# Performance work log

Measured on AMD Instinct MI355X. Metric: run time of the kernel, lower is better.

Reference implementation:

```python
import jax, jax.numpy as jnp
import numpy as np

HID = 512
NOISE = 128
VOCAB = 5000
BATCH = 256
STEPS = 64
EPS = 1e-5
SOS = VOCAB - 1

def lrelu(x):
    return jnp.where(x >= 0, x, 0.2 * x)

def batchnorm(x, gamma, beta):
    # training-mode BatchNorm1d: batch statistics, biased variance
    mu = jnp.mean(x, axis=0)
    var = jnp.mean((x - mu) ** 2, axis=0)
    return gamma * (x - mu) / jnp.sqrt(var + EPS) + beta

def gru_cell(x, h, w_ih, w_hh, b_ih, b_hh):
    gi = x @ w_ih.T + b_ih  # [B, 3H]
    gh = h @ w_hh.T + b_hh
    i_r, i_z, i_n = jnp.split(gi, 3, axis=1)
    h_r, h_z, h_n = jnp.split(gh, 3, axis=1)
    r = jax.nn.sigmoid(i_r + h_r)
    zg = jax.nn.sigmoid(i_z + h_z)
    n = jnp.tanh(i_n + r * h_n)
    return (1.0 - zg) * n + zg * h

def setup_inputs() -> dict:
    key = jax.random.key(0)
    ks = jax.random.split(key, 12)
    s = lambda fi, fo: 1.0 / np.sqrt(fi)
    u = lambda k, shp, b: jax.random.uniform(k, shp, jnp.float32, -b, b)
    return {
        "z": jax.random.normal(ks[0], (BATCH, NOISE), jnp.float32),
        "z2h_w": u(ks[1], (HID, NOISE), s(NOISE, HID)),
        "z2h_b": u(ks[2], (HID,), s(NOISE, HID)),
        "emb": jax.random.normal(ks[3], (VOCAB, HID), jnp.float32),
        "bn1_g": jnp.ones((HID,), jnp.float32), "bn1_b": jnp.zeros((HID,), jnp.float32),
        "bn2_g": jnp.ones((2 * HID,), jnp.float32), "bn2_b": jnp.zeros((2 * HID,), jnp.float32),
        "bn3_g": jnp.ones((HID,), jnp.float32), "bn3_b": jnp.zeros((HID,), jnp.float32),
        "gru_wih": u(ks[4], (3 * HID, 2 * HID), s(HID, 0)),
        "gru_whh": u(ks[5], (3 * HID, HID), s(HID, 0)),
        "gru_bih": u(ks[6], (3 * HID,), s(HID, 0)),
        "gru_bhh": u(ks[7], (3 * HID,), s(HID, 0)),
        "h2o_w": u(ks[8], (VOCAB, HID), s(HID, 0)),
        "h2o_b": u(ks[9], (VOCAB,), s(HID, 0)),
        "gumbel_u": jax.random.uniform(ks[10], (STEPS, BATCH, VOCAB), jnp.float32),
        "num_steps": STEPS,
        "temperature": 0.8,
    }

def reference(z, z2h_w, z2h_b, emb, bn1_g, bn1_b, bn2_g, bn2_b, bn3_g, bn3_b,
              gru_wih, gru_whh, gru_bih, gru_bhh, h2o_w, h2o_b, gumbel_u,
              num_steps, temperature):
    z0 = batchnorm(lrelu(z @ z2h_w.T + z2h_b), bn1_g, bn1_b)  # [B, H]
    h0 = z0
    prev0 = jnp.full((z.shape[0],), SOS, jnp.int32)

    def step(carry, u_t):
        h, prev = carry
        e = lrelu(emb[prev])                                   # [B, H]
        si = batchnorm(jnp.concatenate([e, z0], axis=1), bn2_g, bn2_b)
        h = gru_cell(si, h, gru_wih, gru_whh, gru_bih, gru_bhh)
        o = batchnorm(lrelu(h), bn3_g, bn3_b)
        logits = o @ h2o_w.T + h2o_b                           # [B, V]
        g = -jnp.log(-jnp.log(u_t + 1e-20) + 1e-20)            # gumbel noise
        y = jax.nn.softmax((logits + g) / temperature, axis=-1)
        prev = jnp.argmax(y, axis=-1).astype(jnp.int32)
        return (h, prev), y

    _, ys = jax.lax.scan(step, (h0, prev0), gumbel_u[:num_steps])
    return jnp.transpose(ys, (1, 0, 2))  # [B, steps, V]
```

## Files before the change

kernel.cpp:

```cpp
#include <hip/hip_runtime.h>
#include <math.h>

#define HH 512
#define BB 256
#define NK 128

__device__ __forceinline__ float lrelu(float x){ return x >= 0.f ? x : 0.2f*x; }
__device__ __forceinline__ float sigm(float x){ return 1.f/(1.f+expf(-x)); }

__device__ __forceinline__ float blk_sum(float v, float* red){
  int t = threadIdx.x;
  red[t] = v; __syncthreads();
  #pragma unroll
  for (int s = 128; s > 0; s >>= 1){
    if (t < s) red[t] += red[t+s];
    __syncthreads();
  }
  float r = red[0]; __syncthreads();
  return r;
}

__global__ __launch_bounds__(256) void k_init(
    const float* __restrict__ z, const float* __restrict__ w, const float* __restrict__ bz,
    const float* __restrict__ g1, const float* __restrict__ b1,
    const float* __restrict__ g2, const float* __restrict__ b2,
    float* __restrict__ h0, float* __restrict__ sz0, int* __restrict__ prev, int sos)
{
  __shared__ float red[256];
  int j = blockIdx.x, i = threadIdx.x;
  const float4* zr = (const float4*)(z + i*NK);
  const float4* wr = (const float4*)(w + j*NK);
  float acc = bz[j];
  #pragma unroll 8
  for (int k = 0; k < NK/4; k++){
    float4 a = zr[k], b = wr[k];
    acc = fmaf(a.x, b.x, acc); acc = fmaf(a.y, b.y, acc);
    acc = fmaf(a.z, b.z, acc); acc = fmaf(a.w, b.w, acc);
  }
  float t = lrelu(acc);
  float mu  = blk_sum(t, red) * (1.f/BB);
  float d   = t - mu;
  float var = blk_sum(d*d, red) * (1.f/BB);
  float z0v = g1[j] * d / sqrtf(var + 1e-5f) + b1[j];
  h0[i*HH + j] = z0v;
  float mu2  = blk_sum(z0v, red) * (1.f/BB);
  float d2   = z0v - mu2;
  float var2 = blk_sum(d2*d2, red) * (1.f/BB);
  sz0[i*HH + j] = g2[HH + j] * d2 / sqrtf(var2 + 1e-5f) + b2[HH + j];
  if (j == 0) prev[i] = sos;
}

__global__ __launch_bounds__(256) void k_embed(
    const int* __restrict__ prev, const float* __restrict__ emb,
    const float* __restrict__ g2, const float* __restrict__ b2,
    float* __restrict__ se)
{
  __shared__ float red[256];
  int j = blockIdx.x, i = threadIdx.x;
  float t = lrelu(emb[prev[i]*HH + j]);
  float mu  = blk_sum(t, red) * (1.f/BB);
  float d   = t - mu;
  float var = blk_sum(d*d, red) * (1.f/BB);
  se[i*HH + j] = g2[j] * d / sqrtf(var + 1e-5f) + b2[j];
}

__global__ __launch_bounds__(256) void k_bn3(
    const float* __restrict__ h, const float* __restrict__ g3, const float* __restrict__ b3,
    float* __restrict__ o)
{
  __shared__ float red[256];
  int j = blockIdx.x, i = threadIdx.x;
  float t = lrelu(h[i*HH + j]);
  float mu  = blk_sum(t, red) * (1.f/BB);
  float d   = t - mu;
  float var = blk_sum(d*d, red) * (1.f/BB);
  o[i*HH + j] = g3[j] * d / sqrtf(var + 1e-5f) + b3[j];
}

#define KT 64
__global__ __launch_bounds__(256) void k_gru(
    const float* __restrict__ se, const float* __restrict__ hcur,
    const float* __restrict__ wih, const float* __restrict__ whh,
    const float* __restrict__ gz0, const float* __restrict__ bhh,
    float* __restrict__ hnext)
{
  __shared__ float sA[2][32][68];
  __shared__ float sB[6][16][68];
  int m0 = blockIdx.x*32, kc0 = blockIdx.y*16;
  int tl = threadIdx.x;
  float accI[3][2] = {{0,0},{0,0},{0,0}};
  float accH[3][2] = {{0,0},{0,0},{0,0}};
  int c = tl & 15, r2 = (tl >> 4) * 2;

  for (int kt = 0; kt < HH; kt += KT){
    #pragma unroll
    for (int rep = 0; rep < 4; rep++){
      int f = tl + 256*rep;
      int mat = f >> 9; int fi = f & 511;
      int row = fi >> 4; int kq = (fi & 15) * 4;
      const float* src = mat ? hcur : se;
      *(float4*)&sA[mat][row][kq] = *(const float4*)&src[(m0+row)*HH + kt + kq];
    }
    #pragma unroll
    for (int rep = 0; rep < 6; rep++){
      int f = tl + 256*rep;
      int m6 = f >> 8; int fi = f & 255;
      int row = fi >> 4; int kq = (fi & 15) * 4;
      int gate = (m6 < 3) ? m6 : m6 - 3;
      int n = gate*HH + kc0 + row;
      float4 v;
      if (m6 < 3) v = *(const float4*)&wih[n*1024 + kt + kq];
      else        v = *(const float4*)&whh[n*HH   + kt + kq];
      *(float4*)&sB[m6][row][kq] = v;
    }
    __syncthreads();
    #pragma unroll
    for (int kk = 0; kk < KT; kk += 4){
      float4 a0 = *(const float4*)&sA[0][r2  ][kk];
      float4 a1 = *(const float4*)&sA[0][r2+1][kk];
      float4 h0v = *(const float4*)&sA[1][r2  ][kk];
      float4 h1v = *(const float4*)&sA[1][r2+1][kk];
      #pragma unroll
      for (int g = 0; g < 3; g++){
        float4 we = *(const float4*)&sB[g][c][kk];
        accI[g][0] = fmaf(a0.x,we.x, fmaf(a0.y,we.y, fmaf(a0.z,we.z, fmaf(a0.w,we.w, accI[g][0]))));
        accI[g][1] = fmaf(a1.x,we.x, fmaf(a1.y,we.y, fmaf(a1.z,we.z, fmaf(a1.w,we.w, accI[g][1]))));
        float4 wh = *(const float4*)&sB[3+g][c][kk];
        accH[g][0] = fmaf(h0v.x,wh.x, fmaf(h0v.y,wh.y, fmaf(h0v.z,wh.z, fmaf(h0v.w,wh.w, accH[g][0]))));
        accH[g][1] = fmaf(h1v.x,wh.x, fmaf(h1v.y,wh.y, fmaf(h1v.z,wh.z, fmaf(h1v.w,wh.w, accH[g][1]))));
      }
    }
    __syncthreads();
  }
  int k = kc0 + c;
  #pragma unroll
  for (int r = 0; r < 2; r++){
    int i = m0 + r2 + r;
    float gir = accI[0][r] + gz0[i*1536 + k];
    float giz = accI[1][r] + gz0[i*1536 + 512 + k];
    float gin = accI[2][r] + gz0[i*1536 + 1024 + k];
    float ghr = accH[0][r] + bhh[k];
    float ghz = accH[1][r] + bhh[512 + k];
    float ghn = accH[2][r] + bhh[1024 + k];
    float rg = sigm(gir + ghr);
    float zg = sigm(giz + ghz);
    float ng = tanhf(gin + rg*ghn);
    float hv = hcur[i*HH + k];
    hnext[i*HH + k] = (1.f - zg)*ng + zg*hv;
  }
}

__global__ __launch_bounds__(256) void k_mm(
    const float* __restrict__ A, int lda,
    const float* __restrict__ Bm, int ldb,
    const float* __restrict__ bias, int N,
    float* __restrict__ out, int ldc,
    int mode,
    const float* __restrict__ gum, int ldg,
    const float* __restrict__ temp)
{
  __shared__ float sA[32][68];
  __shared__ float sB[64][68];
  int m0 = blockIdx.x*32, n0 = blockIdx.y*64;
  int tl = threadIdx.x;
  float acc[4][2] = {{0,0},{0,0},{0,0},{0,0}};
  int c1 = tl & 31, r4 = (tl >> 5) * 4;

  for (int kt = 0; kt < HH; kt += 64){
    #pragma unroll
    for (int rep = 0; rep < 2; rep++){
      int f = tl + 256*rep; int row = f >> 4; int kq = (f & 15) * 4;
      *(float4*)&sA[row][kq] = *(const float4*)&A[(m0+row)*lda + kt + kq];
    }
    #pragma unroll
    for (int rep = 0; rep < 4; rep++){
      int f = tl + 256*rep; int row = f >> 4; int kq = (f & 15) * 4;
      float4 v = make_float4(0.f,0.f,0.f,0.f);
      if (n0 + row < N) v = *(const float4*)&Bm[(n0+row)*ldb + kt + kq];
      *(float4*)&sB[row][kq] = v;
    }
    __syncthreads();
    #pragma unroll
    for (int kk = 0; kk < 64; kk += 4){
      float4 b0 = *(const float4*)&sB[c1     ][kk];
      float4 b1 = *(const float4*)&sB[c1 + 32][kk];
      #pragma unroll
      for (int r = 0; r < 4; r++){
        float4 a = *(const float4*)&sA[r4+r][kk];
        acc[r][0] = fmaf(a.x,b0.x, fmaf(a.y,b0.y, fmaf(a.z,b0.z, fmaf(a.w,b0.w, acc[r][0]))));
        acc[r][1] = fmaf(a.x,b1.x, fmaf(a.y,b1.y, fmaf(a.z,b1.z, fmaf(a.w,b1.w, acc[r][1]))));
      }
    }
    __syncthreads();
  }

  if (mode == 0){
    #pragma unroll
    for (int r = 0; r < 4; r++)
      #pragma unroll
      for (int j = 0; j < 2; j++){
        int v = n0 + c1 + 32*j;
        if (v < N) out[(m0+r4+r)*ldc + v] = acc[r][j] + bias[v];
      }
  } else {
    float tv = temp[0];
    #pragma unroll
    for (int r = 0; r < 4; r++)
      #pragma unroll
      for (int j = 0; j < 2; j++){
        int v = n0 + c1 + 32*j;
        if (v < N){
          int i = m0 + r4 + r;
          float u = gum[i*ldg + v];
          float g = -logf(-logf(u + 1e-20f) + 1e-20f);
          out[i*ldc + v] = (acc[r][j] + bias[v] + g) / tv;
        }
      }
  }
}

__global__ __launch_bounds__(256) void k_softmax(
    float* __restrict__ outrow, int ldc, int V, int* __restrict__ prev)
{
  __shared__ float sbuf[5000];
  __shared__ float rmax[256];
  __shared__ int   ridx[256];
  __shared__ float rsum[256];
  int i = blockIdx.x, t = threadIdx.x;
  float* row = outrow + (long)i*ldc;
  float bm = -3.4e38f; int bi = 0;
  for (int v = t; v < V; v += 256){
    float s = row[v]; sbuf[v] = s;
    if (s > bm){ bm = s; bi = v; }
  }
  rmax[t] = bm; ridx[t] = bi; __syncthreads();
  for (int s = 128; s > 0; s >>= 1){
    if (t < s){
      float mv = rmax[t+s]; int mi = ridx[t+s];
      if (mv > rmax[t] || (mv == rmax[t] && mi < ridx[t])){ rmax[t] = mv; ridx[t] = mi; }
    }
    __syncthreads();
  }
  float m = rmax[0];
  float ls = 0.f;
  for (int v = t; v < V; v += 256){
    float p = expf(sbuf[v] - m); sbuf[v] = p; ls += p;
  }
  rsum[t] = ls; __syncthreads();
  for (int s = 128; s > 0; s >>= 1){
    if (t < s) rsum[t] += rsum[t+s];
    __syncthreads();
  }
  float inv = 1.f / rsum[0];
  for (int v = t; v < V; v += 256) row[v] = sbuf[v] * inv;
  if (t == 0) prev[i] = ridx[0];
}

extern "C" void kernel_launch(void* const* d_in, const int* in_sizes, int n_in,
                              void* d_out, int out_size, void* d_ws, size_t ws_size,
                              hipStream_t stream)
{
  const float* z     = (const float*)d_in[0];
  const float* z2h_w = (const float*)d_in[1];
  const float* z2h_b = (const float*)d_in[2];
  const float* emb   = (const float*)d_in[3];
  const float* bn1_g = (const float*)d_in[4];
  const float* bn1_b = (const float*)d_in[5];
  const float* bn2_g = (const float*)d_in[6];
  const float* bn2_b = (const float*)d_in[7];
  const float* bn3_g = (const float*)d_in[8];
  const float* bn3_b = (const float*)d_in[9];
  const float* wih   = (const float*)d_in[10];
  const float* whh   = (const float*)d_in[11];
  const float* bih   = (const float*)d_in[12];
  const float* bhh   = (const float*)d_in[13];
  const float* h2o_w = (const float*)d_in[14];
  const float* h2o_b = (const float*)d_in[15];
  const float* gum   = (const float*)d_in[16];
  const float* temp  = (const float*)d_in[18];
  float* out = (float*)d_out;

  int V = in_sizes[15];
  int steps = out_size / (BB * V);

  char* ws = (char*)d_ws;
  float* sz0 = (float*)ws;  ws += (size_t)BB*HH*4;
  float* gz0 = (float*)ws;  ws += (size_t)BB*3*HH*4;
  float* se  = (float*)ws;  ws += (size_t)BB*HH*4;
  float* hb0 = (float*)ws;  ws += (size_t)BB*HH*4;
  float* hb1 = (float*)ws;  ws += (size_t)BB*HH*4;
  float* ob  = (float*)ws;  ws += (size_t)BB*HH*4;
  int*   prev = (int*)ws;

  k_init<<<HH, 256, 0, stream>>>(z, z2h_w, z2h_b, bn1_g, bn1_b, bn2_g, bn2_b,
                                 hb0, sz0, prev, V - 1);
  k_mm<<<dim3(BB/32, (3*HH)/64), 256, 0, stream>>>(
      sz0, HH, wih + HH, 2*HH, bih, 3*HH, gz0, 3*HH, 0, nullptr, 0, nullptr);

  for (int t = 0; t < steps; t++){
    const float* hc = (t & 1) ? hb1 : hb0;
    float*       hn = (t & 1) ? hb0 : hb1;
    k_embed<<<HH, 256, 0, stream>>>(prev, emb, bn2_g, bn2_b, se);
    k_gru<<<dim3(BB/32, HH/16), 256, 0, stream>>>(se, hc, wih, whh, gz0, bhh, hn);
    k_bn3<<<HH, 256, 0, stream>>>(hn, bn3_g, bn3_b, ob);
    k_mm<<<dim3(BB/32, (V + 63)/64), 256, 0, stream>>>(
        ob, HH, h2o_w, HH, h2o_b, V,
        out + (size_t)t*V, steps*V, 1, gum + (size_t)t*BB*V, V, temp);
    k_softmax<<<BB, 256, 0, stream>>>(out + (size_t)t*V, steps*V, V, prev);
  }
}
```

Measured before the change: 6.834 ms.

## Fuse embed-BN, GRU cell and output BN into one kernel; retile logits GEMM

Replaces the per-step embed/BN2, GRU and BN3 kernels with one kernel. Each block owns two hidden columns across the whole batch, so the batch statistics for both batchnorms are computed in-block and the intermediate se buffer and two launches go away. The logits GEMM is retiled so each block covers all 256 rows against 20 vocab columns, with vectorized Gumbel/temperature epilogue stores. The cost is that each fused block re-reads all embedding rows and the full hidden state, and the kernels run only 256 or 250 blocks with large LDS footprints, which limits occupancy. Variance is now computed as E[x^2]-mu^2, which is less numerically stable.

```diff
diff --git a/kernel.cpp b/kernel.cpp
--- a/kernel.cpp
+++ b/kernel.cpp
@@ -18,6 +18,12 @@
   }
   float r = red[0]; __syncthreads();
   return r;
+}
+
+__device__ __forceinline__ float wave_sum(float v){
+  #pragma unroll
+  for (int m = 32; m >= 1; m >>= 1) v += __shfl_xor(v, m, 64);
+  return v;
 }
 
 __global__ __launch_bounds__(256) void k_init(
@@ -50,114 +56,11 @@
   if (j == 0) prev[i] = sos;
 }
 
-__global__ __launch_bounds__(256) void k_embed(
-    const int* __restrict__ prev, const float* __restrict__ emb,
-    const float* __restrict__ g2, const float* __restrict__ b2,
-    float* __restrict__ se)
-{
-  __shared__ float red[256];
-  int j = blockIdx.x, i = threadIdx.x;
-  float t = lrelu(emb[prev[i]*HH + j]);
-  float mu  = blk_sum(t, red) * (1.f/BB);
-  float d   = t - mu;
-  float var = blk_sum(d*d, red) * (1.f/BB);
-  se[i*HH + j] = g2[j] * d / sqrtf(var + 1e-5f) + b2[j];
-}
-
-__global__ __launch_bounds__(256) void k_bn3(
-    const float* __restrict__ h, const float* __restrict__ g3, const float* __restrict__ b3,
-    float* __restrict__ o)
-{
-  __shared__ float red[256];
-  int j = blockIdx.x, i = threadIdx.x;
-  float t = lrelu(h[i*HH + j]);
-  float mu  = blk_sum(t, red) * (1.f/BB);
-  float d   = t - mu;
-  float var = blk_sum(d*d, red) * (1.f/BB);
-  o[i*HH + j] = g3[j] * d / sqrtf(var + 1e-5f) + b3[j];
-}
-
-#define KT 64
-__global__ __launch_bounds__(256) void k_gru(
-    const float* __restrict__ se, const float* __restrict__ hcur,
-    const float* __restrict__ wih, const float* __restrict__ whh,
-    const float* __restrict__ gz0, const float* __restrict__ bhh,
-    float* __restrict__ hnext)
-{
-  __shared__ float sA[2][32][68];
-  __shared__ float sB[6][16][68];
-  int m0 = blockIdx.x*32, kc0 = blockIdx.y*16;
-  int tl = threadIdx.x;
-  float accI[3][2] = {{0,0},{0,0},{0,0}};
-  float accH[3][2] = {{0,0},{0,0},{0,0}};
-  int c = tl & 15, r2 = (tl >> 4) * 2;
-
-  for (int kt = 0; kt < HH; kt += KT){
-    #pragma unroll
-    for (int rep = 0; rep < 4; rep++){
-      int f = tl + 256*rep;
-      int mat = f >> 9; int fi = f & 511;
-      int row = fi >> 4; int kq = (fi & 15) * 4;
-      const float* src = mat ? hcur : se;
-      *(float4*)&sA[mat][row][kq] = *(const float4*)&src[(m0+row)*HH + kt + kq];
-    }
-    #pragma unroll
-    for (int rep = 0; rep < 6; rep++){
-      int f = tl + 256*rep;
-      int m6 = f >> 8; int fi = f & 255;
-      int row = fi >> 4; int kq = (fi & 15) * 4;
-      int gate = (m6 < 3) ? m6 : m6 - 3;
-      int n = gate*HH + kc0 + row;
-      float4 v;
-      if (m6 < 3) v = *(const float4*)&wih[n*1024 + kt + kq];
-      else        v = *(const float4*)&whh[n*HH   + kt + kq];
-      *(float4*)&sB[m6][row][kq] = v;
-    }
-    __syncthreads();
-    #pragma unroll
-    for (int kk = 0; kk < KT; kk += 4){
-      float4 a0 = *(const float4*)&sA[0][r2  ][kk];
-      float4 a1 = *(const float4*)&sA[0][r2+1][kk];
-      float4 h0v = *(const float4*)&sA[1][r2  ][kk];
-      float4 h1v = *(const float4*)&sA[1][r2+1][kk];
-      #pragma unroll
-      for (int g = 0; g < 3; g++){
-        float4 we = *(const float4*)&sB[g][c][kk];
-        accI[g][0] = fmaf(a0.x,we.x, fmaf(a0.y,we.y, fmaf(a0.z,we.z, fmaf(a0.w,we.w, accI[g][0]))));
-        accI[g][1] = fmaf(a1.x,we.x, fmaf(a1.y,we.y, fmaf(a1.z,we.z, fmaf(a1.w,we.w, accI[g][1]))));
-        float4 wh = *(const float4*)&sB[3+g][c][kk];
-        accH[g][0] = fmaf(h0v.x,wh.x, fmaf(h0v.y,wh.y, fmaf(h0v.z,wh.z, fmaf(h0v.w,wh.w, accH[g][0]))));
-        accH[g][1] = fmaf(h1v.x,wh.x, fmaf(h1v.y,wh.y, fmaf(h1v.z,wh.z, fmaf(h1v.w,wh.w, accH[g][1]))));
-      }
-    }
-    __syncthreads();
-  }
-  int k = kc0 + c;
-  #pragma unroll
-  for (int r = 0; r < 2; r++){
-    int i = m0 + r2 + r;
-    float gir = accI[0][r] + gz0[i*1536 + k];
-    float giz = accI[1][r] + gz0[i*1536 + 512 + k];
-    float gin = accI[2][r] + gz0[i*1536 + 1024 + k];
-    float ghr = accH[0][r] + bhh[k];
-    float ghz = accH[1][r] + bhh[512 + k];
-    float ghn = accH[2][r] + bhh[1024 + k];
-    float rg = sigm(gir + ghr);
-    float zg = sigm(giz + ghz);
-    float ng = tanhf(gin + rg*ghn);
-    float hv = hcur[i*HH + k];
-    hnext[i*HH + k] = (1.f - zg)*ng + zg*hv;
-  }
-}
-
 __global__ __launch_bounds__(256) void k_mm(
     const float* __restrict__ A, int lda,
     const float* __restrict__ Bm, int ldb,
     const float* __restrict__ bias, int N,
-    float* __restrict__ out, int ldc,
-    int mode,
-    const float* __restrict__ gum, int ldg,
-    const float* __restrict__ temp)
+    float* __restrict__ out, int ldc)
 {
   __shared__ float sA[32][68];
   __shared__ float sB[64][68];
@@ -193,29 +96,224 @@
     }
     __syncthreads();
   }
-
-  if (mode == 0){
-    #pragma unroll
-    for (int r = 0; r < 4; r++)
+  #pragma unroll
+  for (int r = 0; r < 4; r++)
+    #pragma unroll
+    for (int j = 0; j < 2; j++){
+      int v = n0 + c1 + 32*j;
+      if (v < N) out[(m0+r4+r)*ldc + v] = acc[r][j] + bias[v];
+    }
+}
+
+__global__ __launch_bounds__(256) void k_gru2(
+    const int*   __restrict__ prev, const float* __restrict__ emb,
+    const float* __restrict__ g2,   const float* __restrict__ b2,
+    const float* __restrict__ wih,  const float* __restrict__ whh,
+    const float* __restrict__ hcur, const float* __restrict__ gz0,
+    const float* __restrict__ bhh,
+    const float* __restrict__ g3,   const float* __restrict__ b3,
+    float* __restrict__ hnext, float* __restrict__ o_out)
+{
+  __shared__ float  sE[256*65];
+  __shared__ float2 pstat[256*4];
+  __shared__ float  sBW[64*12];
+  __shared__ float2 ssc[64];
+  __shared__ float2 wst[4][2];
+
+  const int tid = threadIdx.x;
+  const int w = tid >> 6, l = tid & 63;
+  const int rq = l >> 4, m4 = (l & 15) * 4;
+  const int c0 = blockIdx.x * 2;
+
+  float aR0=0.f,aR1=0.f,aZ0=0.f,aZ1=0.f,aNI0=0.f,aNI1=0.f,aNH0=0.f,aNH1=0.f;
+
+  for (int kt = 0; kt < HH; kt += 64){
+    float s0=0.f,s1=0.f,s2=0.f,s3=0.f,q0=0.f,q1=0.f,q2=0.f,q3=0.f;
+    #pragma unroll
+    for (int i = 0; i < 16; i++){
+      int row = w*64 + i*4 + rq;
+      int e = prev[row];
+      float4 v = *(const float4*)&emb[(size_t)e*HH + kt + m4];
+      float4 t; t.x=lrelu(v.x); t.y=lrelu(v.y); t.z=lrelu(v.z); t.w=lrelu(v.w);
+      *(float4*)&sE[row*65 + m4] = t;
+      s0+=t.x; q0+=t.x*t.x; s1+=t.y; q1+=t.y*t.y;
+      s2+=t.z; q2+=t.z*t.z; s3+=t.w; q3+=t.w*t.w;
+    }
+    *(float4*)&pstat[tid*4]     = make_float4(s0,q0,s1,q1);
+    *(float4*)&pstat[tid*4 + 2] = make_float4(s2,q2,s3,q3);
+    #pragma unroll
+    for (int m = w; m < 6; m += 4){
+      int g = m >> 1, c = m & 1;
+      int n = g*HH + c0 + c;
+      sBW[l*12 + m] = wih[n*(2*HH) + kt + l];
+    }
+    __syncthreads();
+    if (tid < 64){
+      int mi = tid >> 2, sub = tid & 3;
+      float S = 0.f, Q = 0.f;
       #pragma unroll
-      for (int j = 0; j < 2; j++){
-        int v = n0 + c1 + 32*j;
-        if (v < N) out[(m0+r4+r)*ldc + v] = acc[r][j] + bias[v];
-      }
+      for (int ww = 0; ww < 4; ww++)
+        #pragma unroll
+        for (int r2 = 0; r2 < 4; r2++){
+          float2 p = pstat[(ww*64 + r2*16 + mi)*4 + sub];
+          S += p.x; Q += p.y;
+        }
+      float mu  = S * (1.f/BB);
+      float var = Q * (1.f/BB) - mu*mu;
+      float sc  = g2[kt + tid] * rsqrtf(var + 1e-5f);
+      ssc[tid] = make_float2(sc, b2[kt + tid] - mu*sc);
+    }
+    __syncthreads();
+    #pragma unroll 4
+    for (int kk = 0; kk < 64; kk++){
+      float a = sE[tid*65 + kk];
+      float2 ss = ssc[kk];
+      float an = fmaf(a, ss.x, ss.y);
+      float4 b4 = *(const float4*)&sBW[kk*12];
+      float2 bn = *(const float2*)&sBW[kk*12 + 4];
+      aR0  = fmaf(an, b4.x, aR0);  aR1  = fmaf(an, b4.y, aR1);
+      aZ0  = fmaf(an, b4.z, aZ0);  aZ1  = fmaf(an, b4.w, aZ1);
+      aNI0 = fmaf(an, bn.x, aNI0); aNI1 = fmaf(an, bn.y, aNI1);
+    }
+    __syncthreads();
+  }
+
+  for (int kt = 0; kt < HH; kt += 64){
+    #pragma unroll
+    for (int i = 0; i < 16; i++){
+      int row = w*64 + i*4 + rq;
+      float4 v = *(const float4*)&hcur[row*HH + kt + m4];
+      *(float4*)&sE[row*65 + m4] = v;
+    }
+    #pragma unroll
+    for (int m = w; m < 6; m += 4){
+      int g = m >> 1, c = m & 1;
+      int n = g*HH + c0 + c;
+      sBW[l*12 + m] = whh[n*HH + kt + l];
+    }
+    __syncthreads();
+    #pragma unroll 4
+    for (int kk = 0; kk < 64; kk++){
+      float a = sE[tid*65 + kk];
+      float4 b4 = *(const float4*)&sBW[kk*12];
+      float2 bn = *(const float2*)&sBW[kk*12 + 4];
+      aR0  = fmaf(a, b4.x, aR0);  aR1  = fmaf(a, b4.y, aR1);
+      aZ0  = fmaf(a, b4.z, aZ0);  aZ1  = fmaf(a, b4.w, aZ1);
+      aNH0 = fmaf(a, bn.x, aNH0); aNH1 = fmaf(a, bn.y, aNH1);
+    }
+    __syncthreads();
+  }
+
+  int row = tid;
+  float t3v[2];
+  #pragma unroll
+  for (int c = 0; c < 2; c++){
+    float aR  = c ? aR1  : aR0;
+    float aZ  = c ? aZ1  : aZ0;
+    float aNI = c ? aNI1 : aNI0;
+    float aNH = c ? aNH1 : aNH0;
+    int col = c0 + c;
+    float rg = sigm(aR + bhh[col]      + gz0[row*(3*HH) + col]);
+    float zg = sigm(aZ + bhh[HH + col] + gz0[row*(3*HH) + HH + col]);
+    float ng = tanhf(aNI + gz0[row*(3*HH) + 2*HH + col] + rg*(aNH + bhh[2*HH + col]));
+    float hv = hcur[row*HH + col];
+    float hn = (1.f - zg)*ng + zg*hv;
+    hnext[row*HH + col] = hn;
+    t3v[c] = lrelu(hn);
+  }
+  float S0 = wave_sum(t3v[0]), Q0 = wave_sum(t3v[0]*t3v[0]);
+  float S1 = wave_sum(t3v[1]), Q1 = wave_sum(t3v[1]*t3v[1]);
+  if (l == 0){ wst[w][0] = make_float2(S0, Q0); wst[w][1] = make_float2(S1, Q1); }
+  __syncthreads();
+  #pragma unroll
+  for (int c = 0; c < 2; c++){
+    float S = 0.f, Q = 0.f;
+    #pragma unroll
+    for (int ww = 0; ww < 4; ww++){ float2 p = wst[ww][c]; S += p.x; Q += p.y; }
+    float mu  = S * (1.f/BB);
+    float var = Q * (1.f/BB) - mu*mu;
+    int col = c0 + c;
+    float sc = g3[col] * rsqrtf(var + 1e-5f);
+    float sh = b3[col] - mu*sc;
+    o_out[row*HH + col] = fmaf(t3v[c], sc, sh);
+  }
+}
+
+__global__ __launch_bounds__(256) void k_mm2(
+    const float* __restrict__ A,
+    const float* __restrict__ W,
+    const float* __restrict__ bias, int V,
+    float* __restrict__ outp, int ldc,
+    const float* __restrict__ gum, int ldg,
+    const float* __restrict__ temp)
+{
+  __shared__ float sA[256*65];
+  __shared__ float sB[64*20];
+  const int tid = threadIdx.x;
+  const int w = tid >> 6, l = tid & 63;
+  const int rq = l >> 4, m4 = (l & 15)*4;
+  const int c0 = blockIdx.x * 20;
+
+  float acc[20];
+  #pragma unroll
+  for (int c = 0; c < 20; c++) acc[c] = 0.f;
+
+  for (int kt = 0; kt < HH; kt += 64){
+    #pragma unroll
+    for (int i = 0; i < 16; i++){
+      int row = w*64 + i*4 + rq;
+      float4 v = *(const float4*)&A[row*HH + kt + m4];
+      *(float4*)&sA[row*65 + m4] = v;
+    }
+    #pragma unroll
+    for (int m = w; m < 20; m += 4){
+      int n = c0 + m; if (n >= V) n = V - 1;
+      sB[l*20 + m] = W[(size_t)n*HH + kt + l];
+    }
+    __syncthreads();
+    #pragma unroll 2
+    for (int kk = 0; kk < 64; kk++){
+      float a = sA[tid*65 + kk];
+      float4 B0 = *(const float4*)&sB[kk*20 + 0];
+      float4 B1 = *(const float4*)&sB[kk*20 + 4];
+      float4 B2 = *(const float4*)&sB[kk*20 + 8];
+      float4 B3 = *(const float4*)&sB[kk*20 + 12];
+      float4 B4 = *(const float4*)&sB[kk*20 + 16];
+      acc[0]  = fmaf(a, B0.x, acc[0]);  acc[1]  = fmaf(a, B0.y, acc[1]);
+      acc[2]  = fmaf(a, B0.z, acc[2]);  acc[3]  = fmaf(a, B0.w, acc[3]);
+      acc[4]  = fmaf(a, B1.x, acc[4]);  acc[5]  = fmaf(a, B1.y, acc[5]);
+      acc[6]  = fmaf(a, B1.z, acc[6]);  acc[7]  = fmaf(a, B1.w, acc[7]);
+      acc[8]  = fmaf(a, B2.x, acc[8]);  acc[9]  = fmaf(a, B2.y, acc[9]);
+      acc[10] = fmaf(a, B2.z, acc[10]); acc[11] = fmaf(a, B2.w, acc[11]);
+      acc[12] = fmaf(a, B3.x, acc[12]); acc[13] = fmaf(a, B3.y, acc[13]);
+      acc[14] = fmaf(a, B3.z, acc[14]); acc[15] = fmaf(a, B3.w, acc[15]);
+      acc[16] = fmaf(a, B4.x, acc[16]); acc[17] = fmaf(a, B4.y, acc[17]);
+      acc[18] = fmaf(a, B4.z, acc[18]); acc[19] = fmaf(a, B4.w, acc[19]);
+    }
+    __syncthreads();
+  }
+
+  float invT = 1.f / temp[0];
+  int row = tid;
+  float* op = outp + (size_t)row*ldc + c0;
+  const float* gp = gum + (size_t)row*ldg + c0;
+  if (c0 + 20 <= V){
+    #pragma unroll
+    for (int qd = 0; qd < 5; qd++){
+      float4 u = *(const float4*)&gp[qd*4];
+      float4 r;
+      r.x = (acc[qd*4+0] + bias[c0+qd*4+0] - logf(-logf(u.x + 1e-20f) + 1e-20f)) * invT;
+      r.y = (acc[qd*4+1] + bias[c0+qd*4+1] - logf(-logf(u.y + 1e-20f) + 1e-20f)) * invT;
+      r.z = (acc[qd*4+2] + bias[c0+qd*4+2] - logf(-logf(u.z + 1e-20f) + 1e-20f)) * invT;
+      r.w = (acc[qd*4+3] + bias[c0+qd*4+3] - logf(-logf(u.w + 1e-20f) + 1e-20f)) * invT;
+      *(float4*)&op[qd*4] = r;
+    }
   } else {
-    float tv = temp[0];
-    #pragma unroll
-    for (int r = 0; r < 4; r++)
-      #pragma unroll
-      for (int j = 0; j < 2; j++){
-        int v = n0 + c1 + 32*j;
-        if (v < N){
-          int i = m0 + r4 + r;
-          float u = gum[i*ldg + v];
-          float g = -logf(-logf(u + 1e-20f) + 1e-20f);
-          out[i*ldc + v] = (acc[r][j] + bias[v] + g) / tv;
-        }
-      }
+    for (int c = 0; c < 20; c++){
+      int n = c0 + c; if (n >= V) break;
+      float u = gp[c];
+      op[c] = (acc[c] + bias[n] - logf(-logf(u + 1e-20f) + 1e-20f)) * invT;
+    }
   }
 }
 
@@ -286,7 +384,6 @@
   char* ws = (char*)d_ws;
   float* sz0 = (float*)ws;  ws += (size_t)BB*HH*4;
   float* gz0 = (float*)ws;  ws += (size_t)BB*3*HH*4;
-  float* se  = (float*)ws;  ws += (size_t)BB*HH*4;
   float* hb0 = (float*)ws;  ws += (size_t)BB*HH*4;
   float* hb1 = (float*)ws;  ws += (size_t)BB*HH*4;
   float* ob  = (float*)ws;  ws += (size_t)BB*HH*4;
@@ -295,17 +392,17 @@
   k_init<<<HH, 256, 0, stream>>>(z, z2h_w, z2h_b, bn1_g, bn1_b, bn2_g, bn2_b,
                                  hb0, sz0, prev, V - 1);
   k_mm<<<dim3(BB/32, (3*HH)/64), 256, 0, stream>>>(
-      sz0, HH, wih + HH, 2*HH, bih, 3*HH, gz0, 3*HH, 0, nullptr, 0, nullptr);
-
+      sz0, HH, wih + HH, 2*HH, bih, 3*HH, gz0, 3*HH);
+
+  int mmg = (V + 19) / 20;
   for (int t = 0; t < steps; t++){
     const float* hc = (t & 1) ? hb1 : hb0;
     float*       hn = (t & 1) ? hb0 : hb1;
-    k_embed<<<HH, 256, 0, stream>>>(prev, emb, bn2_g, bn2_b, se);
-    k_gru<<<dim3(BB/32, HH/16), 256, 0, stream>>>(se, hc, wih, whh, gz0, bhh, hn);
-    k_bn3<<<HH, 256, 0, stream>>>(hn, bn3_g, bn3_b, ob);
-    k_mm<<<dim3(BB/32, (V + 63)/64), 256, 0, stream>>>(
-        ob, HH, h2o_w, HH, h2o_b, V,
-        out + (size_t)t*V, steps*V, 1, gum + (size_t)t*BB*V, V, temp);
+    k_gru2<<<HH/2, 256, 0, stream>>>(prev, emb, bn2_g, bn2_b, wih, whh, hc,
+                                     gz0, bhh, bn3_g, bn3_b, hn, ob);
+    k_mm2<<<mmg, 256, 0, stream>>>(ob, h2o_w, h2o_b, V,
+                                   out + (size_t)t*V, steps*V,
+                                   gum + (size_t)t*BB*V, V, temp);
     k_softmax<<<BB, 256, 0, stream>>>(out + (size_t)t*V, steps*V, V, prev);
   }
 }
```

Result: slower. 9.671 ms (+41.5%).
